# Performance work log

Hardware: AMD Instinct MI355X
Metric: run time of the kernel (lower is better)

The kernel has to match this reference:

```python
import math
import jax, jax.numpy as jnp
import numpy as np

N_HEAD = 16
LORA_SCALE = 16.0 / 8.0  # lora_alpha / r


def lora_linear(x, W, b, A, B):
    # y = x @ W^T + b + scale * (x @ A^T) @ B^T
    base = jnp.einsum('btc,oc->bto', x, W) + b
    low = jnp.einsum('btc,rc->btr', x, A)
    return base + LORA_SCALE * jnp.einsum('btr,or->bto', low, B)


def setup_inputs() -> dict:
    key = jax.random.key(0)
    ks = jax.random.split(key, 8)
    B, T, C = 2, 2048, 1024
    r = 8
    s = 0.02
    return {
        'x': jax.random.normal(ks[0], (B, T, C), jnp.float32),
        'W_attn': jax.random.normal(ks[1], (3 * C, C), jnp.float32) * s,
        'b_attn': jnp.zeros((3 * C,), jnp.float32),
        'A_attn': jax.random.normal(ks[2], (r, C), jnp.float32) * s,
        'B_attn': jax.random.normal(ks[3], (3 * C, r), jnp.float32) * s,
        'W_proj': jax.random.normal(ks[4], (C, C), jnp.float32) * s,
        'b_proj': jnp.zeros((C,), jnp.float32),
        'A_proj': jax.random.normal(ks[5], (r, C), jnp.float32) * s,
        'B_proj': jax.random.normal(ks[6], (C, r), jnp.float32) * s,
    }


def reference(x, W_attn, b_attn, A_attn, B_attn, W_proj, b_proj, A_proj, B_proj):
    B, T, C = x.shape
    H = N_HEAD
    hd = C // H
    qkv = lora_linear(x, W_attn, b_attn, A_attn, B_attn)  # [B,T,3C]
    q, k, v = jnp.split(qkv, 3, axis=2)
    # [B,H,T,hd]
    q = q.reshape(B, T, H, hd).transpose(0, 2, 1, 3)
    k = k.reshape(B, T, H, hd).transpose(0, 2, 1, 3)
    v = v.reshape(B, T, H, hd).transpose(0, 2, 1, 3)
    att = jnp.einsum('bhqd,bhkd->bhqk', q, k) * (1.0 / math.sqrt(hd))
    causal = jnp.tril(jnp.ones((T, T), bool))
    att = jnp.where(causal, att, -jnp.inf)
    att = jax.nn.softmax(att, axis=-1)
    out = jnp.einsum('bhqk,bhkd->bhqd', att, v)
    out = out.transpose(0, 2, 1, 3).reshape(B, T, C)
    return lora_linear(out, W_proj, b_proj, A_proj, B_proj)
```

## Files before the change

kernel.cpp:

```cpp
#include <hip/hip_runtime.h>
#include <hip/hip_bf16.h>
#include <stdint.h>

typedef __bf16 bf16_t;
typedef __bf16 bf16x8 __attribute__((ext_vector_type(8)));
typedef __bf16 bf16x4 __attribute__((ext_vector_type(4)));
typedef float f32x4 __attribute__((ext_vector_type(4)));
typedef uint32_t u32;

typedef __attribute__((address_space(1))) void as1void;
typedef __attribute__((address_space(3))) void as3void;

#define LOG2E 1.44269504088896340736f

__device__ __forceinline__ void gll16(const void* g, void* l) {
  __builtin_amdgcn_global_load_lds((as1void*)g, (as3void*)l, 16, 0, 0);
}

__global__ void prep_weff(const float* __restrict__ W,
                          const float* __restrict__ Bm,
                          const float* __restrict__ Am,
                          bf16_t* __restrict__ Weff, int OC) {
  int idx = blockIdx.x * 256 + threadIdx.x;
  if (idx >= OC) return;
  int o = idx >> 10, c = idx & 1023;
  float acc = W[idx];
#pragma unroll
  for (int r = 0; r < 8; ++r)
    acc += 2.0f * Bm[o * 8 + r] * Am[r * 1024 + c];
  Weff[idx] = (bf16_t)acc;
}

__global__ void cast_bf4(const float4* __restrict__ X, bf16x4* __restrict__ Xb, int n4) {
  int i = blockIdx.x * 256 + threadIdx.x;
  if (i < n4) {
    float4 v = X[i];
    bf16x4 o = {(bf16_t)v.x, (bf16_t)v.y, (bf16_t)v.z, (bf16_t)v.w};
    Xb[i] = o;
  }
}

template <bool QKV>
__global__ __launch_bounds__(256, 3) void gemm_bt(
    const bf16_t* __restrict__ A, const bf16_t* __restrict__ Bt,
    const float* __restrict__ bias,
    bf16_t* __restrict__ Qb, bf16_t* __restrict__ Kb, bf16_t* __restrict__ Vb,
    float* __restrict__ Out) {
  __shared__ bf16_t Als[128][64];
  __shared__ bf16_t Bls[128][64];
  const int m0 = blockIdx.x * 128;
  const int n0 = blockIdx.y * 128;
  const int tid = threadIdx.x;
  const int lane = tid & 63;
  const int w = tid >> 6;
  const int wm = w >> 1, wn = w & 1;
  const int lr = lane & 15, g = lane >> 4;
  const int sw = (lane & 7) << 3;
  const int srow = lane >> 3;
  const int soff = ((lane & 7) ^ srow) * 8;

  f32x4 acc[4][4] = {};

  for (int k0 = 0; k0 < 1024; k0 += 64) {
#pragma unroll
    for (int c = 0; c < 4; ++c) {
      int r = w * 32 + c * 8 + srow;
      gll16(A + (size_t)(m0 + r) * 1024 + k0 + soff, &Als[w * 32 + c * 8][0]);
      gll16(Bt + (size_t)(n0 + r) * 1024 + k0 + soff, &Bls[w * 32 + c * 8][0]);
    }
    __syncthreads();
#pragma unroll
    for (int ks = 0; ks < 2; ++ks) {
      bf16x8 af[4], bfv[4];
#pragma unroll
      for (int i = 0; i < 4; ++i)
        af[i] = *(const bf16x8*)&Als[wm * 64 + i * 16 + lr][(ks * 32 + g * 8) ^ sw];
#pragma unroll
      for (int j = 0; j < 4; ++j)
        bfv[j] = *(const bf16x8*)&Bls[wn * 64 + j * 16 + lr][(ks * 32 + g * 8) ^ sw];
#pragma unroll
      for (int i = 0; i < 4; ++i)
#pragma unroll
        for (int j = 0; j < 4; ++j)
          acc[i][j] = __builtin_amdgcn_mfma_f32_16x16x32_bf16(af[i], bfv[j], acc[i][j], 0, 0, 0);
    }
    __syncthreads();
  }

#pragma unroll
  for (int i = 0; i < 4; ++i) {
#pragma unroll
    for (int j = 0; j < 4; ++j) {
#pragma unroll
      for (int e = 0; e < 4; ++e) {
        int m = m0 + wm * 64 + i * 16 + g * 4 + e;
        int n = n0 + wn * 64 + j * 16 + lr;
        float v = acc[i][j][e] + bias[n];
        if (QKV) {
          int b = m >> 11, t = m & 2047;
          int which = n >> 10, hn = n & 1023;
          int h = hn >> 6, d = hn & 63;
          bf16_t* dst = (which == 0) ? Qb : (which == 1) ? Kb : Vb;
          dst[(((size_t)(b * 16 + h)) * 2048 + t) * 64 + d] = (bf16_t)v;
        } else {
          Out[(size_t)m * 1024 + n] = v;
        }
      }
    }
  }
}

__global__ __launch_bounds__(512, 4) void attn_fwd(
    const bf16_t* __restrict__ Qb, const bf16_t* __restrict__ Kb,
    const bf16_t* __restrict__ Vb, bf16_t* __restrict__ Ob) {
  __shared__ bf16_t Kls[128][64];
  __shared__ bf16_t Vt[64][128];
  __shared__ bf16_t Pl[8][16][128];

  int id = blockIdx.x;
  int xcd = id & 7, j = id >> 3;
  int lo = j & 31, hi = j >> 5;
  int bh = xcd * 4 + (lo & 3);
  int qb = hi ? 15 - (lo >> 2) : (lo >> 2);
  int b = bh >> 4, h = bh & 15;

  const int tid = threadIdx.x, lane = tid & 63, w = tid >> 6;
  const int grp = w >> 2, wl = w & 3;
  const int g = lane >> 4, lr = lane & 15;
  const int sw = (lane & 7) << 3;
  const bf16_t* Qp = Qb + (size_t)bh * 2048 * 64;
  const bf16_t* Kp = Kb + (size_t)bh * 2048 * 64;
  const bf16_t* Vp = Vb + (size_t)bh * 2048 * 64;
  const float sc = 0.125f * LOG2E;

  const int q0 = qb * 128;
  const int qrow = q0 + grp * 64 + wl * 16 + lr;

  bf16x8 qf0, qf1;
  {
    const bf16_t* qsrc = Qp + (size_t)qrow * 64 + g * 8;
    qf0 = *(const bf16x8*)(qsrc);
    qf1 = *(const bf16x8*)(qsrc + 32);
  }

  int vkey[4];
#pragma unroll
  for (int fc2 = 0; fc2 < 4; ++fc2) {
    int d = fc2 * 16 + lr;
    vkey[fc2] = (((d & 7) ^ ((d >> 1) & 7)) << 3);
  }

  const int ksrow = lane >> 3;
  const int ksoff = ((lane & 7) ^ ksrow) * 8;

  float m_run = -3e38f, l_run = 0.f;
  f32x4 oacc[4] = {};
  const int ktiles = qb + 1;

  for (int kt = 0; kt < ktiles; ++kt) {
    const int k0 = kt * 128;
    const bool lastt = (kt == ktiles - 1);
    const int famax = (lastt && grp == 0) ? 4 : 8;
    __syncthreads();

#pragma unroll
    for (int c = 0; c < 2; ++c) {
      int rbase = (w * 2 + c) * 8;
      gll16(Kp + (size_t)(k0 + rbase + ksrow) * 64 + ksoff, &Kls[rbase][0]);
    }

    {
      int kbase = (tid >> 5) * 8;
      int dbase = (tid & 31) * 2;
      u32 rowv[8];
#pragma unroll
      for (int r = 0; r < 8; ++r)
        rowv[r] = *(const u32*)(Vp + (size_t)(k0 + kbase + r) * 64 + dbase);
#pragma unroll
      for (int dd = 0; dd < 2; ++dd) {
        u32 sel = dd ? 0x07060302u : 0x05040100u;
        int4 val;
        val.x = __builtin_amdgcn_perm(rowv[1], rowv[0], sel);
        val.y = __builtin_amdgcn_perm(rowv[3], rowv[2], sel);
        val.z = __builtin_amdgcn_perm(rowv[5], rowv[4], sel);
        val.w = __builtin_amdgcn_perm(rowv[7], rowv[6], sel);
        int d = dbase + dd;
        int key = ((d & 7) ^ ((d >> 1) & 7)) << 3;
        *(int4*)&Vt[d][kbase ^ key] = val;
      }
    }
    __syncthreads();

    f32x4 s[8] = {};
#pragma unroll
    for (int ks = 0; ks < 2; ++ks) {
#pragma unroll
      for (int fa = 0; fa < 8; ++fa) {
        if (fa < famax) {
          bf16x8 kf = *(const bf16x8*)&Kls[fa * 16 + lr][(ks * 32 + g * 8) ^ sw];
          s[fa] = __builtin_amdgcn_mfma_f32_16x16x32_bf16(kf, ks ? qf1 : qf0, s[fa], 0, 0, 0);
        }
      }
    }

    float mloc = -3e38f;
#pragma unroll
    for (int fa = 0; fa < 8; ++fa) {
      if (fa < famax) {
#pragma unroll
        for (int e = 0; e < 4; ++e) {
          float v = s[fa][e] * sc;
          if (lastt) {
            int kk = k0 + fa * 16 + g * 4 + e;
            v = (kk > qrow) ? -3e38f : v;
          }
          s[fa][e] = v;
          mloc = fmaxf(mloc, v);
        }
      }
    }
    mloc = fmaxf(mloc, __shfl_xor(mloc, 16, 64));
    mloc = fmaxf(mloc, __shfl_xor(mloc, 32, 64));
    if (!__all(mloc <= m_run + 8.0f)) {
      float mnew = fmaxf(m_run, mloc);
      float rs = __builtin_amdgcn_exp2f(m_run - mnew);
      m_run = mnew;
      l_run *= rs;
      float rs_e[4];
#pragma unroll
      for (int e = 0; e < 4; ++e) rs_e[e] = __shfl(rs, g * 4 + e, 64);
#pragma unroll
      for (int fc2 = 0; fc2 < 4; ++fc2)
#pragma unroll
        for (int e = 0; e < 4; ++e) oacc[fc2][e] *= rs_e[e];
    }
    float lsum = 0.f;
#pragma unroll
    for (int fa = 0; fa < 8; ++fa) {
      if (fa < famax) {
        float p0 = __builtin_amdgcn_exp2f(s[fa][0] - m_run);
        float p1 = __builtin_amdgcn_exp2f(s[fa][1] - m_run);
        float p2 = __builtin_amdgcn_exp2f(s[fa][2] - m_run);
        float p3 = __builtin_amdgcn_exp2f(s[fa][3] - m_run);
        lsum += (p0 + p1) + (p2 + p3);
        bf16x4 pv = {(bf16_t)p0, (bf16_t)p1, (bf16_t)p2, (bf16_t)p3};
        *(bf16x4*)&Pl[w][lr][(fa * 16 + g * 4) ^ sw] = pv;
      }
    }
    lsum += __shfl_xor(lsum, 16, 64);
    lsum += __shfl_xor(lsum, 32, 64);
    l_run += lsum;

    asm volatile("s_waitcnt lgkmcnt(0)" ::: "memory");
    __builtin_amdgcn_sched_barrier(0);

    const int ks2max = (lastt && grp == 0) ? 2 : 4;
#pragma unroll
    for (int ks2 = 0; ks2 < 4; ++ks2) {
      if (ks2 < ks2max) {
        bf16x8 pa = *(const bf16x8*)&Pl[w][lr][(ks2 * 32 + g * 8) ^ sw];
#pragma unroll
        for (int fc2 = 0; fc2 < 4; ++fc2) {
          bf16x8 vf = *(const bf16x8*)&Vt[fc2 * 16 + lr][(ks2 * 32 + g * 8) ^ vkey[fc2]];
          oacc[fc2] = __builtin_amdgcn_mfma_f32_16x16x32_bf16(pa, vf, oacc[fc2], 0, 0, 0);
        }
      }
    }
  }

  float le[4];
#pragma unroll
  for (int e = 0; e < 4; ++e) le[e] = __shfl(l_run, g * 4 + e, 64);
#pragma unroll
  for (int e = 0; e < 4; ++e) {
    float inv = 1.0f / le[e];
    int t = q0 + grp * 64 + wl * 16 + g * 4 + e;
#pragma unroll
    for (int fc2 = 0; fc2 < 4; ++fc2) {
      int dcol = h * 64 + fc2 * 16 + lr;
      Ob[((size_t)(b * 2048 + t)) * 1024 + dcol] = (bf16_t)(oacc[fc2][e] * inv);
    }
  }
}

extern "C" void kernel_launch(void* const* d_in, const int* in_sizes, int n_in,
                              void* d_out, int out_size, void* d_ws, size_t ws_size,
                              hipStream_t stream) {
  const float* x      = (const float*)d_in[0];
  const float* W_attn = (const float*)d_in[1];
  const float* b_attn = (const float*)d_in[2];
  const float* A_attn = (const float*)d_in[3];
  const float* B_attn = (const float*)d_in[4];
  const float* W_proj = (const float*)d_in[5];
  const float* b_proj = (const float*)d_in[6];
  const float* A_proj = (const float*)d_in[7];
  const float* B_proj = (const float*)d_in[8];
  float* out = (float*)d_out;

  char* ws = (char*)d_ws;
  bf16_t* WaE = (bf16_t*)(ws);
  bf16_t* WpE = (bf16_t*)(ws + 6291456);
  bf16_t* Xb  = (bf16_t*)(ws + 8388608);
  bf16_t* Qb  = (bf16_t*)(ws + 16777216);
  bf16_t* Kb  = (bf16_t*)(ws + 25165824);
  bf16_t* Vb  = (bf16_t*)(ws + 33554432);
  bf16_t* Ob  = (bf16_t*)(ws + 41943040);

  prep_weff<<<12288, 256, 0, stream>>>(W_attn, B_attn, A_attn, WaE, 3072 * 1024);
  prep_weff<<<4096, 256, 0, stream>>>(W_proj, B_proj, A_proj, WpE, 1024 * 1024);
  cast_bf4<<<4096, 256, 0, stream>>>((const float4*)x, (bf16x4*)Xb, 1048576);

  gemm_bt<true><<<dim3(32, 24), 256, 0, stream>>>(Xb, WaE, b_attn, Qb, Kb, Vb, nullptr);
  attn_fwd<<<512, 512, 0, stream>>>(Qb, Kb, Vb, Ob);
  gemm_bt<false><<<dim3(32, 8), 256, 0, stream>>>(Ob, WpE, b_proj, nullptr, nullptr, nullptr, out);
}
```

Baseline: 114.2 us.

## Rewrite attention with 32x32 MFMA, register-resident P, and merged weight prep

New measurement: 118.2 us. 1.03x slower.

```diff
diff --git a/kernel.cpp b/kernel.cpp
--- a/kernel.cpp
+++ b/kernel.cpp
@@ -5,8 +5,11 @@
 typedef __bf16 bf16_t;
 typedef __bf16 bf16x8 __attribute__((ext_vector_type(8)));
 typedef __bf16 bf16x4 __attribute__((ext_vector_type(4)));
+typedef __bf16 bf16x2 __attribute__((ext_vector_type(2)));
 typedef float f32x4 __attribute__((ext_vector_type(4)));
+typedef float f32x16 __attribute__((ext_vector_type(16)));
 typedef uint32_t u32;
+typedef uint32_t u32x4 __attribute__((ext_vector_type(4)));
 
 typedef __attribute__((address_space(1))) void as1void;
 typedef __attribute__((address_space(3))) void as3void;
@@ -17,18 +20,30 @@
   __builtin_amdgcn_global_load_lds((as1void*)g, (as3void*)l, 16, 0, 0);
 }
 
-__global__ void prep_weff(const float* __restrict__ W,
-                          const float* __restrict__ Bm,
-                          const float* __restrict__ Am,
-                          bf16_t* __restrict__ Weff, int OC) {
+__device__ __forceinline__ u32 pack2(float a, float b) {
+  bf16x2 t = {(bf16_t)a, (bf16_t)b};
+  return __builtin_bit_cast(u32, t);
+}
+
+__global__ void prep_weff2(const float* __restrict__ W_attn, const float* __restrict__ B_attn,
+                           const float* __restrict__ A_attn, const float* __restrict__ W_proj,
+                           const float* __restrict__ B_proj, const float* __restrict__ A_proj,
+                           bf16_t* __restrict__ WaE, bf16_t* __restrict__ WpE) {
   int idx = blockIdx.x * 256 + threadIdx.x;
-  if (idx >= OC) return;
+  const float *W, *Bm, *Am;
+  bf16_t* dst;
+  if (idx < 3145728) {
+    W = W_attn; Bm = B_attn; Am = A_attn; dst = WaE;
+  } else {
+    idx -= 3145728;
+    W = W_proj; Bm = B_proj; Am = A_proj; dst = WpE;
+  }
   int o = idx >> 10, c = idx & 1023;
   float acc = W[idx];
 #pragma unroll
   for (int r = 0; r < 8; ++r)
     acc += 2.0f * Bm[o * 8 + r] * Am[r * 1024 + c];
-  Weff[idx] = (bf16_t)acc;
+  dst[idx] = (bf16_t)acc;
 }
 
 __global__ void cast_bf4(const float4* __restrict__ X, bf16x4* __restrict__ Xb, int n4) {
@@ -110,175 +125,173 @@
   }
 }
 
-__global__ __launch_bounds__(512, 4) void attn_fwd(
+__global__ __launch_bounds__(256, 2) void attn_fwd(
     const bf16_t* __restrict__ Qb, const bf16_t* __restrict__ Kb,
     const bf16_t* __restrict__ Vb, bf16_t* __restrict__ Ob) {
   __shared__ bf16_t Kls[128][64];
   __shared__ bf16_t Vt[64][128];
-  __shared__ bf16_t Pl[8][16][128];
 
   int id = blockIdx.x;
   int xcd = id & 7, j = id >> 3;
-  int lo = j & 31, hi = j >> 5;
+  int lo = j & 31, hi2 = j >> 5;
   int bh = xcd * 4 + (lo & 3);
-  int qb = hi ? 15 - (lo >> 2) : (lo >> 2);
+  int qb = hi2 ? 15 - (lo >> 2) : (lo >> 2);
   int b = bh >> 4, h = bh & 15;
 
   const int tid = threadIdx.x, lane = tid & 63, w = tid >> 6;
-  const int grp = w >> 2, wl = w & 3;
-  const int g = lane >> 4, lr = lane & 15;
-  const int sw = (lane & 7) << 3;
+  const int q32 = lane & 31;
+  const int hi = lane >> 5;
+  const int ksw = (q32 & 7) << 3;
+  const int vkey = ((q32 & 7) ^ (q32 >> 2)) << 3;
   const bf16_t* Qp = Qb + (size_t)bh * 2048 * 64;
   const bf16_t* Kp = Kb + (size_t)bh * 2048 * 64;
   const bf16_t* Vp = Vb + (size_t)bh * 2048 * 64;
   const float sc = 0.125f * LOG2E;
 
   const int q0 = qb * 128;
-  const int qrow = q0 + grp * 64 + wl * 16 + lr;
-
-  bf16x8 qf0, qf1;
-  {
-    const bf16_t* qsrc = Qp + (size_t)qrow * 64 + g * 8;
-    qf0 = *(const bf16x8*)(qsrc);
-    qf1 = *(const bf16x8*)(qsrc + 32);
-  }
-
-  int vkey[4];
-#pragma unroll
-  for (int fc2 = 0; fc2 < 4; ++fc2) {
-    int d = fc2 * 16 + lr;
-    vkey[fc2] = (((d & 7) ^ ((d >> 1) & 7)) << 3);
-  }
-
-  const int ksrow = lane >> 3;
-  const int ksoff = ((lane & 7) ^ ksrow) * 8;
+  const int qrow = q0 + w * 32 + q32;
+
+  bf16x8 qf[4];
+#pragma unroll
+  for (int ds = 0; ds < 4; ++ds)
+    qf[ds] = *(const bf16x8*)(Qp + (size_t)qrow * 64 + ds * 16 + hi * 8);
 
   float m_run = -3e38f, l_run = 0.f;
-  f32x4 oacc[4] = {};
+  f32x16 o_acc[2] = {};
   const int ktiles = qb + 1;
 
   for (int kt = 0; kt < ktiles; ++kt) {
     const int k0 = kt * 128;
     const bool lastt = (kt == ktiles - 1);
-    const int famax = (lastt && grp == 0) ? 4 : 8;
+    const int nfa = lastt ? (w + 1) : 4;
     __syncthreads();
 
 #pragma unroll
-    for (int c = 0; c < 2; ++c) {
-      int rbase = (w * 2 + c) * 8;
-      gll16(Kp + (size_t)(k0 + rbase + ksrow) * 64 + ksoff, &Kls[rbase][0]);
+    for (int c = 0; c < 4; ++c) {
+      int rb = w * 32 + c * 8;
+      gll16(Kp + (size_t)(k0 + rb + (lane >> 3)) * 64 + ((lane & 7) ^ (lane >> 3)) * 8,
+            &Kls[rb][0]);
     }
 
     {
-      int kbase = (tid >> 5) * 8;
-      int dbase = (tid & 31) * 2;
-      u32 rowv[8];
+      int kbase = (tid >> 4) * 8;
+      int dbase = (tid & 15) * 4;
+      uint2 rowv[8];
 #pragma unroll
       for (int r = 0; r < 8; ++r)
-        rowv[r] = *(const u32*)(Vp + (size_t)(k0 + kbase + r) * 64 + dbase);
-#pragma unroll
-      for (int dd = 0; dd < 2; ++dd) {
-        u32 sel = dd ? 0x07060302u : 0x05040100u;
+        rowv[r] = *(const uint2*)(Vp + (size_t)(k0 + kbase + r) * 64 + dbase);
+#pragma unroll
+      for (int dd = 0; dd < 4; ++dd) {
+        u32 sel = (dd & 1) ? 0x07060302u : 0x05040100u;
+        u32 a0 = (dd >> 1) ? rowv[0].y : rowv[0].x;
+        u32 a1 = (dd >> 1) ? rowv[1].y : rowv[1].x;
+        u32 a2 = (dd >> 1) ? rowv[2].y : rowv[2].x;
+        u32 a3 = (dd >> 1) ? rowv[3].y : rowv[3].x;
+        u32 a4 = (dd >> 1) ? rowv[4].y : rowv[4].x;
+        u32 a5 = (dd >> 1) ? rowv[5].y : rowv[5].x;
+        u32 a6 = (dd >> 1) ? rowv[6].y : rowv[6].x;
+        u32 a7 = (dd >> 1) ? rowv[7].y : rowv[7].x;
         int4 val;
-        val.x = __builtin_amdgcn_perm(rowv[1], rowv[0], sel);
-        val.y = __builtin_amdgcn_perm(rowv[3], rowv[2], sel);
-        val.z = __builtin_amdgcn_perm(rowv[5], rowv[4], sel);
-        val.w = __builtin_amdgcn_perm(rowv[7], rowv[6], sel);
+        val.x = __builtin_amdgcn_perm(a1, a0, sel);
+        val.y = __builtin_amdgcn_perm(a3, a2, sel);
+        val.z = __builtin_amdgcn_perm(a5, a4, sel);
+        val.w = __builtin_amdgcn_perm(a7, a6, sel);
         int d = dbase + dd;
-        int key = ((d & 7) ^ ((d >> 1) & 7)) << 3;
+        int key = ((d & 7) ^ ((d >> 2) & 7)) << 3;
         *(int4*)&Vt[d][kbase ^ key] = val;
       }
     }
     __syncthreads();
 
-    f32x4 s[8] = {};
-#pragma unroll
-    for (int ks = 0; ks < 2; ++ks) {
-#pragma unroll
-      for (int fa = 0; fa < 8; ++fa) {
-        if (fa < famax) {
-          bf16x8 kf = *(const bf16x8*)&Kls[fa * 16 + lr][(ks * 32 + g * 8) ^ sw];
-          s[fa] = __builtin_amdgcn_mfma_f32_16x16x32_bf16(kf, ks ? qf1 : qf0, s[fa], 0, 0, 0);
+    f32x16 s[4] = {};
+#pragma unroll
+    for (int fa = 0; fa < 4; ++fa) {
+      if (fa < nfa) {
+#pragma unroll
+        for (int ds = 0; ds < 4; ++ds) {
+          bf16x8 kf = *(const bf16x8*)&Kls[fa * 32 + q32][(ds * 16 + hi * 8) ^ ksw];
+          s[fa] = __builtin_amdgcn_mfma_f32_32x32x16_bf16(kf, qf[ds], s[fa], 0, 0, 0);
         }
       }
     }
 
     float mloc = -3e38f;
 #pragma unroll
-    for (int fa = 0; fa < 8; ++fa) {
-      if (fa < famax) {
-#pragma unroll
-        for (int e = 0; e < 4; ++e) {
-          float v = s[fa][e] * sc;
-          if (lastt) {
-            int kk = k0 + fa * 16 + g * 4 + e;
-            v = (kk > qrow) ? -3e38f : v;
+    for (int fa = 0; fa < 4; ++fa) {
+      if (fa < nfa) {
+#pragma unroll
+        for (int r = 0; r < 16; ++r) {
+          float v = s[fa][r] * sc;
+          if (lastt && fa == w) {
+            int km = (r & 3) + 8 * (r >> 2) + 4 * hi;
+            if (km > q32) v = -3e38f;
           }
-          s[fa][e] = v;
+          s[fa][r] = v;
           mloc = fmaxf(mloc, v);
         }
       }
     }
-    mloc = fmaxf(mloc, __shfl_xor(mloc, 16, 64));
     mloc = fmaxf(mloc, __shfl_xor(mloc, 32, 64));
     if (!__all(mloc <= m_run + 8.0f)) {
       float mnew = fmaxf(m_run, mloc);
       float rs = __builtin_amdgcn_exp2f(m_run - mnew);
       m_run = mnew;
       l_run *= rs;
-      float rs_e[4];
-#pragma unroll
-      for (int e = 0; e < 4; ++e) rs_e[e] = __shfl(rs, g * 4 + e, 64);
-#pragma unroll
-      for (int fc2 = 0; fc2 < 4; ++fc2)
-#pragma unroll
-        for (int e = 0; e < 4; ++e) oacc[fc2][e] *= rs_e[e];
-    }
+      o_acc[0] *= rs;
+      o_acc[1] *= rs;
+    }
+
     float lsum = 0.f;
 #pragma unroll
-    for (int fa = 0; fa < 8; ++fa) {
-      if (fa < famax) {
-        float p0 = __builtin_amdgcn_exp2f(s[fa][0] - m_run);
-        float p1 = __builtin_amdgcn_exp2f(s[fa][1] - m_run);
-        float p2 = __builtin_amdgcn_exp2f(s[fa][2] - m_run);
-        float p3 = __builtin_amdgcn_exp2f(s[fa][3] - m_run);
-        lsum += (p0 + p1) + (p2 + p3);
-        bf16x4 pv = {(bf16_t)p0, (bf16_t)p1, (bf16_t)p2, (bf16_t)p3};
-        *(bf16x4*)&Pl[w][lr][(fa * 16 + g * 4) ^ sw] = pv;
-      }
-    }
-    lsum += __shfl_xor(lsum, 16, 64);
+    for (int fa = 0; fa < 4; ++fa) {
+      if (fa < nfa) {
+        float p[16];
+#pragma unroll
+        for (int r = 0; r < 16; ++r) {
+          p[r] = __builtin_amdgcn_exp2f(s[fa][r] - m_run);
+          lsum += p[r];
+        }
+        u32 x0 = pack2(p[0], p[1]),   x1 = pack2(p[2], p[3]);
+        u32 x2 = pack2(p[4], p[5]),   x3 = pack2(p[6], p[7]);
+        u32 y0 = pack2(p[8], p[9]),   y1 = pack2(p[10], p[11]);
+        u32 y2 = pack2(p[12], p[13]), y3 = pack2(p[14], p[15]);
+        u32 z0 = hi ? x0 : x2;
+        u32 z1 = hi ? x1 : x3;
+        u32 z2 = hi ? y0 : y2;
+        u32 z3 = hi ? y1 : y3;
+        z0 = (u32)__shfl_xor((int)z0, 32, 64);
+        z1 = (u32)__shfl_xor((int)z1, 32, 64);
+        z2 = (u32)__shfl_xor((int)z2, 32, 64);
+        z3 = (u32)__shfl_xor((int)z3, 32, 64);
+        u32x4 pw0 = hi ? (u32x4){z0, z1, x2, x3} : (u32x4){x0, x1, z0, z1};
+        u32x4 pw1 = hi ? (u32x4){z2, z3, y2, y3} : (u32x4){y0, y1, z2, z3};
+        bf16x8 P0 = __builtin_bit_cast(bf16x8, pw0);
+        bf16x8 P1 = __builtin_bit_cast(bf16x8, pw1);
+#pragma unroll
+        for (int db = 0; db < 2; ++db) {
+          int d = db * 32 + q32;
+          bf16x8 vf0 = *(const bf16x8*)&Vt[d][(fa * 32 + hi * 8) ^ vkey];
+          o_acc[db] = __builtin_amdgcn_mfma_f32_32x32x16_bf16(vf0, P0, o_acc[db], 0, 0, 0);
+          bf16x8 vf1 = *(const bf16x8*)&Vt[d][(fa * 32 + 16 + hi * 8) ^ vkey];
+          o_acc[db] = __builtin_amdgcn_mfma_f32_32x32x16_bf16(vf1, P1, o_acc[db], 0, 0, 0);
+        }
+      }
+    }
     lsum += __shfl_xor(lsum, 32, 64);
     l_run += lsum;
-
-    asm volatile("s_waitcnt lgkmcnt(0)" ::: "memory");
-    __builtin_amdgcn_sched_barrier(0);
-
-    const int ks2max = (lastt && grp == 0) ? 2 : 4;
-#pragma unroll
-    for (int ks2 = 0; ks2 < 4; ++ks2) {
-      if (ks2 < ks2max) {
-        bf16x8 pa = *(const bf16x8*)&Pl[w][lr][(ks2 * 32 + g * 8) ^ sw];
-#pragma unroll
-        for (int fc2 = 0; fc2 < 4; ++fc2) {
-          bf16x8 vf = *(const bf16x8*)&Vt[fc2 * 16 + lr][(ks2 * 32 + g * 8) ^ vkey[fc2]];
-          oacc[fc2] = __builtin_amdgcn_mfma_f32_16x16x32_bf16(pa, vf, oacc[fc2], 0, 0, 0);
-        }
-      }
-    }
-  }
-
-  float le[4];
-#pragma unroll
-  for (int e = 0; e < 4; ++e) le[e] = __shfl(l_run, g * 4 + e, 64);
-#pragma unroll
-  for (int e = 0; e < 4; ++e) {
-    float inv = 1.0f / le[e];
-    int t = q0 + grp * 64 + wl * 16 + g * 4 + e;
-#pragma unroll
-    for (int fc2 = 0; fc2 < 4; ++fc2) {
-      int dcol = h * 64 + fc2 * 16 + lr;
-      Ob[((size_t)(b * 2048 + t)) * 1024 + dcol] = (bf16_t)(oacc[fc2][e] * inv);
+  }
+
+  float inv = 1.0f / l_run;
+  bf16_t* obase = Ob + ((size_t)(b * 2048 + qrow)) * 1024 + h * 64;
+#pragma unroll
+  for (int db = 0; db < 2; ++db) {
+#pragma unroll
+    for (int rg = 0; rg < 4; ++rg) {
+      bf16x4 ov = {(bf16_t)(o_acc[db][rg * 4 + 0] * inv),
+                   (bf16_t)(o_acc[db][rg * 4 + 1] * inv),
+                   (bf16_t)(o_acc[db][rg * 4 + 2] * inv),
+                   (bf16_t)(o_acc[db][rg * 4 + 3] * inv)};
+      *(bf16x4*)(obase + db * 32 + rg * 8 + hi * 4) = ov;
     }
   }
 }
@@ -306,11 +319,10 @@
   bf16_t* Vb  = (bf16_t*)(ws + 33554432);
   bf16_t* Ob  = (bf16_t*)(ws + 41943040);
 
-  prep_weff<<<12288, 256, 0, stream>>>(W_attn, B_attn, A_attn, WaE, 3072 * 1024);
-  prep_weff<<<4096, 256, 0, stream>>>(W_proj, B_proj, A_proj, WpE, 1024 * 1024);
+  prep_weff2<<<16384, 256, 0, stream>>>(W_attn, B_attn, A_attn, W_proj, B_proj, A_proj, WaE, WpE);
   cast_bf4<<<4096, 256, 0, stream>>>((const float4*)x, (bf16x4*)Xb, 1048576);
 
   gemm_bt<true><<<dim3(32, 24), 256, 0, stream>>>(Xb, WaE, b_attn, Qb, Kb, Vb, nullptr);
-  attn_fwd<<<512, 512, 0, stream>>>(Qb, Kb, Vb, Ob);
+  attn_fwd<<<512, 256, 0, stream>>>(Qb, Kb, Vb, Ob);
   gemm_bt<false><<<dim3(32, 8), 256, 0, stream>>>(Ob, WpE, b_proj, nullptr, nullptr, nullptr, out);
 }
```
